# Kernel optimization log

Hardware: AMD Instinct MI355X
Metric: run time of the kernel (lower is better)

## Reference

```python
import jax, jax.numpy as jnp
import numpy as np

N, E, G = 50000, 800000, 128      # nodes, edges, graphs
IN, H, OUT = 128, 128, 2          # feature dims
K, L = 3, 3                       # Chebyshev order, num conv layers
EPS = 1e-5


def setup_inputs() -> dict:
    key = jax.random.key(0)
    ks = jax.random.split(key, 10)
    x = jax.random.normal(ks[0], (N, IN), dtype=jnp.float32)
    edge_index = jax.random.randint(ks[1], (2, E), 0, N, dtype=jnp.int64)
    batch = jnp.sort(jax.random.randint(ks[2], (N,), 0, G, dtype=jnp.int64))
    w_in = jax.random.normal(ks[3], (IN, H), dtype=jnp.float32) * 0.05
    b_in = jnp.zeros((H,), jnp.float32)
    ln_g = jnp.ones((H,), jnp.float32)
    ln_b = jnp.zeros((H,), jnp.float32)
    cheb_w = jax.random.normal(ks[4], (L, K, H, H), dtype=jnp.float32) * 0.05
    cheb_b = jnp.zeros((L, H), jnp.float32)
    bn_g = jnp.ones((L, H), jnp.float32)
    bn_b = jnp.zeros((L, H), jnp.float32)
    w1 = jax.random.normal(ks[5], (H, H // 2), dtype=jnp.float32) * 0.05
    b1 = jnp.zeros((H // 2,), jnp.float32)
    w2 = jax.random.normal(ks[6], (H // 2, OUT), dtype=jnp.float32) * 0.05
    b2 = jnp.zeros((OUT,), jnp.float32)
    return dict(x=x, w_in=w_in, b_in=b_in, ln_g=ln_g, ln_b=ln_b,
                cheb_w=cheb_w, cheb_b=cheb_b, bn_g=bn_g, bn_b=bn_b,
                w1=w1, b1=b1, w2=w2, b2=b2,
                edge_index=edge_index, batch=batch)


def reference(x, w_in, b_in, ln_g, ln_b, cheb_w, cheb_b, bn_g, bn_b,
              w1, b1, w2, b2, edge_index, batch):
    src, dst = edge_index[0], edge_index[1]

    # ChebConv scaled Laplacian with lambda_max=2, sym norm:
    # L_hat = -D^{-1/2} A D^{-1/2}  (self-loop terms cancel in PyG's __norm__)
    deg = jax.ops.segment_sum(jnp.ones((E,), x.dtype), src, num_segments=N)
    dinv = jnp.where(deg > 0, jax.lax.rsqrt(jnp.maximum(deg, 1.0)), 0.0)
    w_edge = -dinv[src] * dinv[dst]  # [E]

    def spmm(h):  # y_i = sum_{(j->i)} w_edge * h_j
        return jax.ops.segment_sum(w_edge[:, None] * h[src], dst, num_segments=N)

    # node_embed: Linear -> LayerNorm -> ReLU (dropout p used in eval => identity)
    h = x @ w_in + b_in
    mu = h.mean(-1, keepdims=True)
    var = h.var(-1, keepdims=True)
    h = (h - mu) * jax.lax.rsqrt(var + EPS) * ln_g + ln_b
    h = jax.nn.relu(h)

    hiddens = [h]
    for l in range(L):
        # Chebyshev recurrence: T0 = h, T1 = L_hat h, Tk = 2 L_hat T_{k-1} - T_{k-2}
        tx0 = h
        out = tx0 @ cheb_w[l, 0]
        tx1 = spmm(tx0)
        out = out + tx1 @ cheb_w[l, 1]
        for k in range(2, K):
            tx2 = 2.0 * spmm(tx1) - tx0
            out = out + tx2 @ cheb_w[l, k]
            tx0, tx1 = tx1, tx2
        out = out + cheb_b[l]
        # BatchNorm1d over nodes (training-mode batch statistics, biased var)
        m = out.mean(0)
        v = out.var(0)
        out = (out - m) * jax.lax.rsqrt(v + EPS) * bn_g[l] + bn_b[l]
        h = jax.nn.relu(out)
        hiddens.append(h)

    # Laplacian (Dirichlet) regularization over all hidden states
    reg = jnp.float32(0.0)
    for hh in hiddens:
        diff = hh[src] - hh[dst]              # [E, H]
        reg = reg + jnp.mean(jnp.sum(diff * diff, axis=-1))
    reg = reg / len(hiddens)

    # global mean pool over batch assignment
    counts = jax.ops.segment_sum(jnp.ones((N,), x.dtype), batch, num_segments=G)
    gsum = jax.ops.segment_sum(h, batch, num_segments=G)
    gmean = gsum / jnp.maximum(counts, 1.0)[:, None]

    z = jax.nn.relu(gmean @ w1 + b1)
    logits = z @ w2 + b2
    return logits, reg
```

## Files before the change

### kernel.cpp

```cpp
#include <hip/hip_runtime.h>
#include <hip/hip_bf16.h>

#define NNODES 50000
#define NEDGES 800000
#define NGRAPH 128
#define EPSV 1e-5f

typedef __attribute__((ext_vector_type(8))) short bf16x8;
typedef __attribute__((ext_vector_type(8))) unsigned short us16x8;
typedef __attribute__((ext_vector_type(4))) float f32x4;
typedef __attribute__((ext_vector_type(2))) float f32x2;

__device__ __forceinline__ unsigned short f2bf(float f) {
    unsigned u = __float_as_uint(f);
    return (unsigned short)((u + 0x7fffu + ((u >> 16) & 1u)) >> 16);
}
__device__ __forceinline__ float bf2f(unsigned short h) {
    return __uint_as_float(((unsigned)h) << 16);
}
__device__ __forceinline__ unsigned pk4_fp8(float a, float b, float c, float d) {
    int w = __builtin_amdgcn_cvt_pk_fp8_f32(a, b, 0, false);
    w = __builtin_amdgcn_cvt_pk_fp8_f32(c, d, w, true);
    return (unsigned)w;
}

__global__ void deg_kernel(const int* __restrict__ src, const int* __restrict__ dst,
                           int* __restrict__ outdeg, int* __restrict__ indeg, int E) {
    int e = blockIdx.x * blockDim.x + threadIdx.x;
    if (e < E) {
        atomicAdd(&outdeg[src[e]], 1);
        atomicAdd(&indeg[dst[e]], 1);
    }
}

__global__ void scan_part(const int* __restrict__ deg, int* __restrict__ bsum,
                          const int* __restrict__ outdeg, float* __restrict__ dinv, int n) {
    __shared__ int sh[256];
    int t = threadIdx.x, i = blockIdx.x * 256 + t;
    if (i < n) {
        int d = outdeg[i];
        dinv[i] = (d > 0) ? rsqrtf((float)d) : 0.0f;
    }
    sh[t] = (i < n) ? deg[i] : 0;
    __syncthreads();
    for (int off = 128; off > 0; off >>= 1) {
        if (t < off) sh[t] += sh[t + off];
        __syncthreads();
    }
    if (t == 0) bsum[blockIdx.x] = sh[0];
}

__global__ void scan_top(int* __restrict__ bsum, int* __restrict__ total, int nb,
                         const int* __restrict__ batch, int* __restrict__ gstart, int n) {
    __shared__ int sh[256];
    int t = threadIdx.x;
    int v = (t < nb) ? bsum[t] : 0;
    sh[t] = v;
    __syncthreads();
    for (int off = 1; off < 256; off <<= 1) {
        int x = (t >= off) ? sh[t - off] : 0;
        __syncthreads();
        sh[t] += x;
        __syncthreads();
    }
    if (t < nb) bsum[t] = sh[t] - v;
    if (t == nb - 1) total[0] = sh[t];
    if (t <= NGRAPH) {
        int lo = 0, hi = n;
        while (lo < hi) {
            int mid = (lo + hi) >> 1;
            if (batch[mid] < t) lo = mid + 1; else hi = mid;
        }
        gstart[t] = lo;
    }
}

__global__ void scan_apply(const int* __restrict__ deg, const int* __restrict__ bsum,
                           int* __restrict__ row_off, int* __restrict__ cursor, int n) {
    __shared__ int sh[256];
    int t = threadIdx.x, i = blockIdx.x * 256 + t;
    int v = (i < n) ? deg[i] : 0;
    sh[t] = v;
    __syncthreads();
    for (int off = 1; off < 256; off <<= 1) {
        int x = (t >= off) ? sh[t - off] : 0;
        __syncthreads();
        sh[t] += x;
        __syncthreads();
    }
    if (i < n) {
        int r = bsum[blockIdx.x] + sh[t] - v;
        row_off[i] = r;
        cursor[i] = r;
    }
}

__global__ void fill_kernel(const int* __restrict__ src, const int* __restrict__ dst,
                            int* __restrict__ cursor, int* __restrict__ col, int E) {
    int e = blockIdx.x * blockDim.x + threadIdx.x;
    if (e < E) {
        int d = dst[e];
        int pos = atomicAdd(&cursor[d], 1);
        col[pos] = src[e];
    }
}

__global__ void wprep_kernel(const float* __restrict__ w_in, const float* __restrict__ cheb_w,
                             unsigned short* __restrict__ Wsp) {
    int p = blockIdx.x;
    int t = threadIdx.x;
    for (int s8 = 0; s8 < 8; ++s8) {
        int slot = s8 * 256 + t;
        int kc = slot >> 9, ct = (slot >> 6) & 7, lane = slot & 63;
        int q = lane >> 4, nn = lane & 15;
        unsigned short* o = Wsp + ((size_t)p * 2048 + slot) * 16;
#pragma unroll
        for (int j = 0; j < 8; ++j) {
            int k = kc * 32 + q * 8 + j, c = ct * 16 + nn;
            float v;
            if (p == 0) {
                v = w_in[k * 128 + c];
            } else {
                int pl = (p - 1) / 3, kk = (p - 1) % 3;
                v = cheb_w[((size_t)(pl * 3 + kk) * 128 + k) * 128 + c];
                if (kk == 0) v -= cheb_w[((size_t)(pl * 3 + 2) * 128 + k) * 128 + c];
                else if (kk == 2) v *= 2.f;
            }
            unsigned short hi = f2bf(v);
            o[j] = hi;
            o[8 + j] = f2bf(v - bf2f(hi));
        }
    }
}

template <int NPARTS, int EPI, int AF32>
__global__ __launch_bounds__(256) void gemm_mfma(
    const void* __restrict__ A0v, const void* __restrict__ A1v, const void* __restrict__ A2v,
    const unsigned short* __restrict__ Wsp, const float* __restrict__ bias,
    float* __restrict__ outp, unsigned short* __restrict__ out16,
    const float* __restrict__ g0, const float* __restrict__ b0,
    float* __restrict__ colsum, float* __restrict__ colsumsq, int n) {
    __shared__ float red[256];
    int t = threadIdx.x, w = t >> 6, l = t & 63;
    int m = l & 15, qk = l >> 4;
    int rowA = blockIdx.x * 64 + w * 16 + m;
    red[t] = 0.f;
    __syncthreads();

    f32x4 acc[8];
#pragma unroll
    for (int ct = 0; ct < 8; ++ct) acc[ct] = (f32x4){0.f, 0.f, 0.f, 0.f};

    bool valid = rowA < n;
#pragma unroll
    for (int p = 0; p < NPARTS; ++p) {
#pragma unroll
        for (int kc = 0; kc < 4; ++kc) {
            bf16x8 ah, al;
            if (AF32) {
                const float* arow = (const float*)A0v;
                if (p == 1) arow = (const float*)A1v;
                if (p == 2) arow = (const float*)A2v;
                arow += (size_t)rowA * 128;
                float4 x0, x1;
                if (valid) {
                    x0 = *(const float4*)&arow[kc * 32 + qk * 8];
                    x1 = *(const float4*)&arow[kc * 32 + qk * 8 + 4];
                } else {
                    x0 = make_float4(0.f, 0.f, 0.f, 0.f); x1 = x0;
                }
                float xs[8] = {x0.x, x0.y, x0.z, x0.w, x1.x, x1.y, x1.z, x1.w};
#pragma unroll
                for (int j = 0; j < 8; ++j) {
                    unsigned short hi = f2bf(xs[j]);
                    ah[j] = (short)hi;
                    al[j] = (short)f2bf(xs[j] - bf2f(hi));
                }
            } else {
                const unsigned short* arow = (const unsigned short*)A0v;
                if (p == 1) arow = (const unsigned short*)A1v;
                if (p == 2) arow = (const unsigned short*)A2v;
                arow += (size_t)rowA * 128;
                if (valid) ah = *(const bf16x8*)&arow[kc * 32 + qk * 8];
                else ah = (bf16x8){0, 0, 0, 0, 0, 0, 0, 0};
            }
            const unsigned short* wb = Wsp + ((size_t)((p * 4 + kc) * 8) * 64 + l) * 16;
#pragma unroll
            for (int ct = 0; ct < 8; ++ct) {
                bf16x8 bh = *(const bf16x8*)(wb + (size_t)ct * 64 * 16);
                bf16x8 bl = *(const bf16x8*)(wb + (size_t)ct * 64 * 16 + 8);
                acc[ct] = __builtin_amdgcn_mfma_f32_16x16x32_bf16(ah, bh, acc[ct], 0, 0, 0);
                if (AF32)
                    acc[ct] = __builtin_amdgcn_mfma_f32_16x16x32_bf16(al, bh, acc[ct], 0, 0, 0);
                acc[ct] = __builtin_amdgcn_mfma_f32_16x16x32_bf16(ah, bl, acc[ct], 0, 0, 0);
            }
        }
    }

    int rowC0 = blockIdx.x * 64 + w * 16 + qk * 4;
    if (EPI == 0) {
        float rs[4] = {0.f, 0.f, 0.f, 0.f}, rss[4] = {0.f, 0.f, 0.f, 0.f};
#pragma unroll
        for (int ct = 0; ct < 8; ++ct) {
            float b = bias[ct * 16 + m];
#pragma unroll
            for (int j = 0; j < 4; ++j) {
                float v = acc[ct][j] + b;
                acc[ct][j] = v;
                rs[j] += v; rss[j] += v * v;
            }
        }
#pragma unroll
        for (int off = 1; off < 16; off <<= 1) {
#pragma unroll
            for (int j = 0; j < 4; ++j) {
                rs[j] += __shfl_xor(rs[j], off, 64);
                rss[j] += __shfl_xor(rss[j], off, 64);
            }
        }
        float mean[4], rstd[4];
#pragma unroll
        for (int j = 0; j < 4; ++j) {
            mean[j] = rs[j] * (1.f / 128.f);
            float var = rss[j] * (1.f / 128.f) - mean[j] * mean[j];
            rstd[j] = rsqrtf(var + EPSV);
        }
#pragma unroll
        for (int ct = 0; ct < 8; ++ct) {
            int c = ct * 16 + m;
            float gg = g0[c], bb = b0[c];
#pragma unroll
            for (int j = 0; j < 4; ++j) {
                int gr = rowC0 + j;
                if (gr < n) {
                    float x = (acc[ct][j] - mean[j]) * rstd[j] * gg + bb;
                    x = fmaxf(x, 0.f);
                    outp[(size_t)gr * 128 + c] = x;
                    out16[(size_t)gr * 128 + c] = f2bf(x);
                }
            }
        }
    } else {
#pragma unroll
        for (int ct = 0; ct < 8; ++ct) {
            int c = ct * 16 + m;
            float b = bias[c];
            float s = 0.f, ss = 0.f;
#pragma unroll
            for (int j = 0; j < 4; ++j) {
                int gr = rowC0 + j;
                if (gr < n) {
                    float v = acc[ct][j] + b;
                    outp[(size_t)gr * 128 + c] = v;
                    s += v; ss += v * v;
                }
            }
            s += __shfl_xor(s, 16, 64);  ss += __shfl_xor(ss, 16, 64);
            s += __shfl_xor(s, 32, 64);  ss += __shfl_xor(ss, 32, 64);
            if (qk == 0) {
                atomicAdd(&red[c], s);
                atomicAdd(&red[128 + c], ss);
            }
        }
        __syncthreads();
        if (t < 128) {
            atomicAdd(&colsum[t], red[t]);
            atomicAdd(&colsumsq[t], red[128 + t]);
        }
    }
}

template <int MODE>
__global__ void spmm_kernel(const unsigned short* __restrict__ g16,
                            const float* __restrict__ self32,
                            unsigned short* __restrict__ dst16, unsigned char* __restrict__ dst8,
                            const int* __restrict__ row_off, const int* __restrict__ col,
                            const float* __restrict__ dinv,
                            const int* __restrict__ outdeg, const int* __restrict__ indeg,
                            int n, double* __restrict__ norm_slots, double* __restrict__ cross_slots) {
    int w = (int)((blockIdx.x * (unsigned)blockDim.x + threadIdx.x) >> 6);
    if (w >= n) return;
    int lane = threadIdx.x & 63;
    int g = lane >> 4;
    int q = lane & 15;
    int s = row_off[w], e = row_off[w + 1];
    float hi[8];
    float4 a = *(const float4*)&self32[(size_t)w * 128 + q * 8];
    float4 b = *(const float4*)&self32[(size_t)w * 128 + q * 8 + 4];
    hi[0] = a.x; hi[1] = a.y; hi[2] = a.z; hi[3] = a.w;
    hi[4] = b.x; hi[5] = b.y; hi[6] = b.z; hi[7] = b.w;
    float acc[8];
#pragma unroll
    for (int j = 0; j < 8; ++j) acc[j] = 0.f;
    float cr = 0.f;
    for (int base = s; base < e; base += 64) {
        int mm = min(e - base, 64);
        int idx = 0; float dv = 0.f;
        if (lane < mm) { idx = col[base + lane]; dv = dinv[idx]; }
        int iters = (mm + 31) >> 5;
        for (int it = 0; it < iters; ++it) {
            int sb = (it << 5) + (g << 3);
            int jj[8]; float dd[8];
#pragma unroll
            for (int u = 0; u < 8; ++u) {
                jj[u] = __shfl(idx, sb + u, 64);
                dd[u] = __shfl(dv, sb + u, 64);
            }
            us16x8 uu[8];
#pragma unroll
            for (int u = 0; u < 8; ++u) {
                uu[u] = (us16x8){0, 0, 0, 0, 0, 0, 0, 0};
                if (sb + u < mm) uu[u] = *(const us16x8*)&g16[(size_t)jj[u] * 128 + q * 8];
            }
#pragma unroll
            for (int u = 0; u < 8; ++u) {
#pragma unroll
                for (int j = 0; j < 8; ++j) {
                    float v = bf2f(uu[u][j]);
                    if (MODE != 2) acc[j] += dd[u] * v;
                    cr += hi[j] * v;
                }
            }
        }
    }
    if (MODE != 2) {
#pragma unroll
        for (int j = 0; j < 8; ++j) {
            acc[j] += __shfl_xor(acc[j], 16, 64);
            acc[j] += __shfl_xor(acc[j], 32, 64);
        }
        if (g == 0) {
            float di = dinv[w];
            float v[8];
            us16x8 o;
#pragma unroll
            for (int j = 0; j < 8; ++j) { v[j] = -di * acc[j]; o[j] = f2bf(v[j]); }
            *(us16x8*)&dst16[(size_t)w * 128 + q * 8] = o;
            uint2 o8;
            o8.x = pk4_fp8(v[0], v[1], v[2], v[3]);
            o8.y = pk4_fp8(v[4], v[5], v[6], v[7]);
            *(uint2*)&dst8[(size_t)w * 128 + q * 8] = o8;
        }
    }
    {
        float nt = 0.f;
#pragma unroll
        for (int j = 0; j < 8; ++j) nt += hi[j] * hi[j];
        nt *= 0.25f;
        for (int off = 32; off > 0; off >>= 1) {
            cr += __shfl_down(cr, off, 64);
            nt += __shfl_down(nt, off, 64);
        }
        if (lane == 0) {
            int slot = w & 255;
            atomicAdd(&cross_slots[slot], (double)cr);
            atomicAdd(&norm_slots[slot], (double)nt * (double)(outdeg[w] + indeg[w]));
        }
    }
}

__global__ void spmm8_kernel(const unsigned char* __restrict__ g8,
                             unsigned short* __restrict__ dst16,
                             const int* __restrict__ row_off, const int* __restrict__ col,
                             const float* __restrict__ dinv, int n) {
    int w = (int)((blockIdx.x * (unsigned)blockDim.x + threadIdx.x) >> 6);
    if (w >= n) return;
    int lane = threadIdx.x & 63;
    int g = lane >> 4;
    int q = lane & 15;
    int s = row_off[w], e = row_off[w + 1];
    float acc[8];
#pragma unroll
    for (int j = 0; j < 8; ++j) acc[j] = 0.f;
    for (int base = s; base < e; base += 64) {
        int mm = min(e - base, 64);
        int idx = 0; float dv = 0.f;
        if (lane < mm) { idx = col[base + lane]; dv = dinv[idx]; }
        int iters = (mm + 31) >> 5;
        for (int it = 0; it < iters; ++it) {
            int sb = (it << 5) + (g << 3);
            int jj[8]; float dd[8];
#pragma unroll
            for (int u = 0; u < 8; ++u) {
                jj[u] = __shfl(idx, sb + u, 64);
                dd[u] = __shfl(dv, sb + u, 64);
            }
            uint2 uu[8];
#pragma unroll
            for (int u = 0; u < 8; ++u) {
                uu[u] = make_uint2(0, 0);
                if (sb + u < mm) uu[u] = *(const uint2*)&g8[(size_t)jj[u] * 128 + q * 8];
            }
#pragma unroll
            for (int u = 0; u < 8; ++u) {
                f32x2 l0 = __builtin_amdgcn_cvt_pk_f32_fp8(uu[u].x, false);
                f32x2 h0 = __builtin_amdgcn_cvt_pk_f32_fp8(uu[u].x, true);
                f32x2 l1 = __builtin_amdgcn_cvt_pk_f32_fp8(uu[u].y, false);
                f32x2 h1 = __builtin_amdgcn_cvt_pk_f32_fp8(uu[u].y, true);
                acc[0] += dd[u] * l0.x; acc[1] += dd[u] * l0.y;
                acc[2] += dd[u] * h0.x; acc[3] += dd[u] * h0.y;
                acc[4] += dd[u] * l1.x; acc[5] += dd[u] * l1.y;
                acc[6] += dd[u] * h1.x; acc[7] += dd[u] * h1.y;
            }
        }
    }
#pragma unroll
    for (int j = 0; j < 8; ++j) {
        acc[j] += __shfl_xor(acc[j], 16, 64);
        acc[j] += __shfl_xor(acc[j], 32, 64);
    }
    if (g == 0) {
        float di = dinv[w];
        us16x8 o;
#pragma unroll
        for (int j = 0; j < 8; ++j) o[j] = f2bf(-di * acc[j]);
        *(us16x8*)&dst16[(size_t)w * 128 + q * 8] = o;
    }
}

__global__ void bnrelu_kernel(const float* __restrict__ outv,
                              const float* __restrict__ colsum, const float* __restrict__ colsumsq,
                              const float* __restrict__ bn_g, const float* __restrict__ bn_b,
                              float* __restrict__ h, unsigned short* __restrict__ h16,
                              int n, int total4) {
    __shared__ float ssc[128], ssh[128];
    int t = threadIdx.x;
    if (t < 128) {
        float m = colsum[t] / (float)n;
        float v = colsumsq[t] / (float)n - m * m;
        float sc = bn_g[t] * rsqrtf(v + EPSV);
        ssc[t] = sc;
        ssh[t] = bn_b[t] - m * sc;
    }
    __syncthreads();
    int i = blockIdx.x * blockDim.x + t;
    if (i >= total4) return;
    float4 o = ((const float4*)outv)[i];
    int c = (i * 4) & 127;
    float4 r;
    r.x = fmaxf(o.x * ssc[c + 0] + ssh[c + 0], 0.f);
    r.y = fmaxf(o.y * ssc[c + 1] + ssh[c + 1], 0.f);
    r.z = fmaxf(o.z * ssc[c + 2] + ssh[c + 2], 0.f);
    r.w = fmaxf(o.w * ssc[c + 3] + ssh[c + 3], 0.f);
    ((float4*)h)[i] = r;
    ushort4 u = make_ushort4(f2bf(r.x), f2bf(r.y), f2bf(r.z), f2bf(r.w));
    ((ushort4*)h16)[i] = u;
}

__global__ void poolmlp_kernel(const float* __restrict__ h, const int* __restrict__ start,
                               const float* __restrict__ w1, const float* __restrict__ b1,
                               const float* __restrict__ w2, const float* __restrict__ b2,
                               const double* __restrict__ norm_slots,
                               const double* __restrict__ cross_slots,
                               float* __restrict__ out) {
    __shared__ float sm[2][128];
    __shared__ float gm[128];
    int g = blockIdx.x, t = threadIdx.x;
    int half = t >> 7, c = t & 127;
    int s = start[g], e = start[g + 1];
    float acc = 0.f;
    for (int r = s + half; r < e; r += 2) acc += h[(size_t)r * 128 + c];
    sm[half][c] = acc;
    __syncthreads();
    if (t < 128) {
        float cnt = fmaxf((float)(e - s), 1.f);
        gm[t] = (sm[0][t] + sm[1][t]) / cnt;
    }
    __syncthreads();
    if (t < 64) {
        float z = b1[t];
        for (int k = 0; k < 128; ++k) z += gm[k] * w1[(size_t)k * 64 + t];
        z = fmaxf(z, 0.f);
        float p0 = z * w2[t * 2 + 0];
        float p1 = z * w2[t * 2 + 1];
        for (int off = 32; off > 0; off >>= 1) {
            p0 += __shfl_down(p0, off, 64);
            p1 += __shfl_down(p1, off, 64);
        }
        if (t == 0) {
            out[g * 2 + 0] = p0 + b2[0];
            out[g * 2 + 1] = p1 + b2[1];
        }
    } else if (g == 0 && t < 128) {
        int l = t - 64;
        double ns = 0.0, cs = 0.0;
        for (int i = l; i < 256; i += 64) { ns += norm_slots[i]; cs += cross_slots[i]; }
        for (int off = 32; off > 0; off >>= 1) {
            ns += __shfl_down(ns, off, 64);
            cs += __shfl_down(cs, off, 64);
        }
        if (l == 0) out[256] = (float)((ns - 2.0 * cs) / ((double)NEDGES * 4.0));
    }
}

extern "C" void kernel_launch(void* const* d_in, const int* in_sizes, int n_in,
                              void* d_out, int out_size, void* d_ws, size_t ws_size,
                              hipStream_t stream) {
    const float* x      = (const float*)d_in[0];
    const float* w_in   = (const float*)d_in[1];
    const float* b_in   = (const float*)d_in[2];
    const float* ln_g   = (const float*)d_in[3];
    const float* ln_b   = (const float*)d_in[4];
    const float* cheb_w = (const float*)d_in[5];
    const float* cheb_b = (const float*)d_in[6];
    const float* bn_g   = (const float*)d_in[7];
    const float* bn_b   = (const float*)d_in[8];
    const float* w1     = (const float*)d_in[9];
    const float* b1     = (const float*)d_in[10];
    const float* w2     = (const float*)d_in[11];
    const float* b2     = (const float*)d_in[12];
    const int*   eidx   = (const int*)d_in[13];
    const int*   batch  = (const int*)d_in[14];
    const int* src = eidx;
    const int* dst = eidx + NEDGES;
    float* out = (float*)d_out;

    char* ws = (char*)d_ws;
    size_t off = 0;
    auto alloc = [&](size_t bytes) -> void* {
        void* p = ws + off;
        off = (off + bytes + 255) & ~(size_t)255;
        return p;
    };
    float* h    = (float*)alloc((size_t)NNODES * 128 * 4);
    float* ob   = (float*)alloc((size_t)NNODES * 128 * 4);
    unsigned short* h16  = (unsigned short*)alloc((size_t)NNODES * 128 * 2);
    unsigned short* t116 = (unsigned short*)alloc((size_t)NNODES * 128 * 2);
    unsigned short* s16  = (unsigned short*)alloc((size_t)NNODES * 128 * 2);
    unsigned char*  t18  = (unsigned char*)alloc((size_t)NNODES * 128);
    unsigned short* Wsp  = (unsigned short*)alloc((size_t)10 * 2048 * 16 * 2);
    int* degs     = (int*)alloc((size_t)2 * NNODES * 4);
    int* outdeg   = degs;
    int* indeg    = degs + NNODES;
    float* dinv   = (float*)alloc((size_t)NNODES * 4);
    int* row_off  = (int*)alloc((size_t)(NNODES + 1) * 4);
    int* cursor   = (int*)alloc((size_t)NNODES * 4);
    int* colv     = (int*)alloc((size_t)NEDGES * 4);
    int* bsum     = (int*)alloc(256 * 4);
    int* gstart   = (int*)alloc((size_t)(NGRAPH + 1) * 4);
    float* colstats = (float*)alloc(256 * 4);
    double* slots   = (double*)alloc(512 * 8);
    double* norm_slots  = slots;
    double* cross_slots = slots + 256;
    float* colsum = colstats, *colsumsq = colstats + 128;

    hipMemsetAsync(degs, 0, (size_t)2 * NNODES * 4, stream);
    hipMemsetAsync(slots, 0, 512 * 8, stream);

    int tE = (NEDGES + 255) / 256;
    int nb = (NNODES + 255) / 256;
    deg_kernel<<<tE, 256, 0, stream>>>(src, dst, outdeg, indeg, NEDGES);
    scan_part<<<nb, 256, 0, stream>>>(indeg, bsum, outdeg, dinv, NNODES);
    scan_top<<<1, 256, 0, stream>>>(bsum, row_off + NNODES, nb, batch, gstart, NNODES);
    scan_apply<<<nb, 256, 0, stream>>>(indeg, bsum, row_off, cursor, NNODES);
    fill_kernel<<<tE, 256, 0, stream>>>(src, dst, cursor, colv, NEDGES);
    wprep_kernel<<<10, 256, 0, stream>>>(w_in, cheb_w, Wsp);

    int gemmBlocks = (NNODES + 63) / 64;
    int waveBlocks = (NNODES * 64 + 255) / 256;
    int total4 = NNODES * 128 / 4;

    gemm_mfma<1, 0, 1><<<gemmBlocks, 256, 0, stream>>>(x, nullptr, nullptr, Wsp, b_in, h, h16,
                                                       ln_g, ln_b, nullptr, nullptr, NNODES);

    for (int l = 0; l < 3; ++l) {
        hipMemsetAsync(colstats, 0, 256 * 4, stream);
        spmm_kernel<0><<<waveBlocks, 256, 0, stream>>>(h16, h, t116, t18, row_off, colv, dinv,
                                                       outdeg, indeg, NNODES, norm_slots, cross_slots);
        spmm8_kernel<<<waveBlocks, 256, 0, stream>>>(t18, s16, row_off, colv, dinv, NNODES);
        gemm_mfma<3, 1, 0><<<gemmBlocks, 256, 0, stream>>>(h16, t116, s16,
            Wsp + (size_t)(1 + 3 * l) * 2048 * 16, cheb_b + (size_t)l * 128, ob, nullptr,
            nullptr, nullptr, colsum, colsumsq, NNODES);
        bnrelu_kernel<<<(total4 + 255) / 256, 256, 0, stream>>>(ob, colsum, colsumsq,
            bn_g + (size_t)l * 128, bn_b + (size_t)l * 128, h, h16, NNODES, total4);
    }
    spmm_kernel<2><<<waveBlocks, 256, 0, stream>>>(h16, h, nullptr, nullptr, row_off, colv, dinv,
                                                   outdeg, indeg, NNODES, norm_slots, cross_slots);

    poolmlp_kernel<<<NGRAPH, 256, 0, stream>>>(h, gstart, w1, b1, w2, b2,
                                               norm_slots, cross_slots, out);
}
```

Before: 848.2 us.

## Gather fp8 hidden states in SpMM, drop fp32 h, pack dinv into CSR

The first SpMM of each layer and the final regularization pass now gather neighbor rows from a new fp8 copy of h instead of bf16, which halves the gather bytes. Both SpMM passes now share one templated kernel. The fp32 copy of h is removed: the self features, pooling and regularization read bf16, and bnrelu writes bf16 plus fp8. The CSR stores (src, dinv[src]) pairs so the dependent dinv lookup goes away, and the per-layer colstats memsets are merged into one. The cost is lower precision in the Chebyshev T1 term and in the Dirichlet regularization, plus an extra repack kernel after the input embedding.

```diff
diff --git a/kernel.cpp b/kernel.cpp
--- a/kernel.cpp
+++ b/kernel.cpp
@@ -96,12 +96,14 @@
 }
 
 __global__ void fill_kernel(const int* __restrict__ src, const int* __restrict__ dst,
-                            int* __restrict__ cursor, int* __restrict__ col, int E) {
+                            const float* __restrict__ dinv,
+                            int* __restrict__ cursor, int2* __restrict__ colw, int E) {
     int e = blockIdx.x * blockDim.x + threadIdx.x;
     if (e < E) {
+        int s = src[e];
         int d = dst[e];
         int pos = atomicAdd(&cursor[d], 1);
-        col[pos] = src[e];
+        colw[pos] = make_int2(s, __float_as_int(dinv[s]));
     }
 }
 
@@ -235,7 +237,6 @@
                 if (gr < n) {
                     float x = (acc[ct][j] - mean[j]) * rstd[j] * gg + bb;
                     x = fmaxf(x, 0.f);
-                    outp[(size_t)gr * 128 + c] = x;
                     out16[(size_t)gr * 128 + c] = f2bf(x);
                 }
             }
@@ -270,14 +271,25 @@
     }
 }
 
+__global__ void repack8_kernel(const unsigned short* __restrict__ h16,
+                               unsigned char* __restrict__ h8, int total8) {
+    int i = blockIdx.x * blockDim.x + threadIdx.x;
+    if (i >= total8) return;
+    us16x8 a = ((const us16x8*)h16)[i];
+    uint2 o;
+    o.x = pk4_fp8(bf2f(a[0]), bf2f(a[1]), bf2f(a[2]), bf2f(a[3]));
+    o.y = pk4_fp8(bf2f(a[4]), bf2f(a[5]), bf2f(a[6]), bf2f(a[7]));
+    ((uint2*)h8)[i] = o;
+}
+
 template <int MODE>
-__global__ void spmm_kernel(const unsigned short* __restrict__ g16,
-                            const float* __restrict__ self32,
-                            unsigned short* __restrict__ dst16, unsigned char* __restrict__ dst8,
-                            const int* __restrict__ row_off, const int* __restrict__ col,
-                            const float* __restrict__ dinv,
-                            const int* __restrict__ outdeg, const int* __restrict__ indeg,
-                            int n, double* __restrict__ norm_slots, double* __restrict__ cross_slots) {
+__global__ void spmm_g(const unsigned char* __restrict__ g8,
+                       const unsigned short* __restrict__ self16,
+                       unsigned short* __restrict__ dst16, unsigned char* __restrict__ dst8,
+                       const int* __restrict__ row_off, const int2* __restrict__ colw,
+                       const float* __restrict__ dinv,
+                       const int* __restrict__ outdeg, const int* __restrict__ indeg,
+                       int n, double* __restrict__ norm_slots, double* __restrict__ cross_slots) {
     int w = (int)((blockIdx.x * (unsigned)blockDim.x + threadIdx.x) >> 6);
     if (w >= n) return;
     int lane = threadIdx.x & 63;
@@ -285,10 +297,11 @@
     int q = lane & 15;
     int s = row_off[w], e = row_off[w + 1];
     float hi[8];
-    float4 a = *(const float4*)&self32[(size_t)w * 128 + q * 8];
-    float4 b = *(const float4*)&self32[(size_t)w * 128 + q * 8 + 4];
-    hi[0] = a.x; hi[1] = a.y; hi[2] = a.z; hi[3] = a.w;
-    hi[4] = b.x; hi[5] = b.y; hi[6] = b.z; hi[7] = b.w;
+    if (MODE != 1) {
+        us16x8 a = *(const us16x8*)&self16[(size_t)w * 128 + q * 8];
+#pragma unroll
+        for (int j = 0; j < 8; ++j) hi[j] = bf2f(a[j]);
+    }
     float acc[8];
 #pragma unroll
     for (int j = 0; j < 8; ++j) acc[j] = 0.f;
@@ -296,7 +309,11 @@
     for (int base = s; base < e; base += 64) {
         int mm = min(e - base, 64);
         int idx = 0; float dv = 0.f;
-        if (lane < mm) { idx = col[base + lane]; dv = dinv[idx]; }
+        if (lane < mm) {
+            int2 cw = colw[base + lane];
+            idx = cw.x;
+            dv = __int_as_float(cw.y);
+        }
         int iters = (mm + 31) >> 5;
         for (int it = 0; it < iters; ++it) {
             int sb = (it << 5) + (g << 3);
@@ -306,19 +323,26 @@
                 jj[u] = __shfl(idx, sb + u, 64);
                 dd[u] = __shfl(dv, sb + u, 64);
             }
-            us16x8 uu[8];
+            uint2 uu[8];
 #pragma unroll
             for (int u = 0; u < 8; ++u) {
-                uu[u] = (us16x8){0, 0, 0, 0, 0, 0, 0, 0};
-                if (sb + u < mm) uu[u] = *(const us16x8*)&g16[(size_t)jj[u] * 128 + q * 8];
+                uu[u] = make_uint2(0, 0);
+                if (sb + u < mm) uu[u] = *(const uint2*)&g8[(size_t)jj[u] * 128 + q * 8];
             }
 #pragma unroll
             for (int u = 0; u < 8; ++u) {
-#pragma unroll
-                for (int j = 0; j < 8; ++j) {
-                    float v = bf2f(uu[u][j]);
-                    if (MODE != 2) acc[j] += dd[u] * v;
-                    cr += hi[j] * v;
+                f32x2 l0 = __builtin_amdgcn_cvt_pk_f32_fp8(uu[u].x, false);
+                f32x2 h0 = __builtin_amdgcn_cvt_pk_f32_fp8(uu[u].x, true);
+                f32x2 l1 = __builtin_amdgcn_cvt_pk_f32_fp8(uu[u].y, false);
+                f32x2 h1 = __builtin_amdgcn_cvt_pk_f32_fp8(uu[u].y, true);
+                float v[8] = {l0.x, l0.y, h0.x, h0.y, l1.x, l1.y, h1.x, h1.y};
+                if (MODE != 2) {
+#pragma unroll
+                    for (int j = 0; j < 8; ++j) acc[j] += dd[u] * v[j];
+                }
+                if (MODE != 1) {
+#pragma unroll
+                    for (int j = 0; j < 8; ++j) cr += hi[j] * v[j];
                 }
             }
         }
@@ -336,13 +360,15 @@
 #pragma unroll
             for (int j = 0; j < 8; ++j) { v[j] = -di * acc[j]; o[j] = f2bf(v[j]); }
             *(us16x8*)&dst16[(size_t)w * 128 + q * 8] = o;
-            uint2 o8;
-            o8.x = pk4_fp8(v[0], v[1], v[2], v[3]);
-            o8.y = pk4_fp8(v[4], v[5], v[6], v[7]);
-            *(uint2*)&dst8[(size_t)w * 128 + q * 8] = o8;
-        }
-    }
-    {
+            if (MODE == 0) {
+                uint2 o8;
+                o8.x = pk4_fp8(v[0], v[1], v[2], v[3]);
+                o8.y = pk4_fp8(v[4], v[5], v[6], v[7]);
+                *(uint2*)&dst8[(size_t)w * 128 + q * 8] = o8;
+            }
+        }
+    }
+    if (MODE != 1) {
         float nt = 0.f;
 #pragma unroll
         for (int j = 0; j < 8; ++j) nt += hi[j] * hi[j];
@@ -359,69 +385,10 @@
     }
 }
 
-__global__ void spmm8_kernel(const unsigned char* __restrict__ g8,
-                             unsigned short* __restrict__ dst16,
-                             const int* __restrict__ row_off, const int* __restrict__ col,
-                             const float* __restrict__ dinv, int n) {
-    int w = (int)((blockIdx.x * (unsigned)blockDim.x + threadIdx.x) >> 6);
-    if (w >= n) return;
-    int lane = threadIdx.x & 63;
-    int g = lane >> 4;
-    int q = lane & 15;
-    int s = row_off[w], e = row_off[w + 1];
-    float acc[8];
-#pragma unroll
-    for (int j = 0; j < 8; ++j) acc[j] = 0.f;
-    for (int base = s; base < e; base += 64) {
-        int mm = min(e - base, 64);
-        int idx = 0; float dv = 0.f;
-        if (lane < mm) { idx = col[base + lane]; dv = dinv[idx]; }
-        int iters = (mm + 31) >> 5;
-        for (int it = 0; it < iters; ++it) {
-            int sb = (it << 5) + (g << 3);
-            int jj[8]; float dd[8];
-#pragma unroll
-            for (int u = 0; u < 8; ++u) {
-                jj[u] = __shfl(idx, sb + u, 64);
-                dd[u] = __shfl(dv, sb + u, 64);
-            }
-            uint2 uu[8];
-#pragma unroll
-            for (int u = 0; u < 8; ++u) {
-                uu[u] = make_uint2(0, 0);
-                if (sb + u < mm) uu[u] = *(const uint2*)&g8[(size_t)jj[u] * 128 + q * 8];
-            }
-#pragma unroll
-            for (int u = 0; u < 8; ++u) {
-                f32x2 l0 = __builtin_amdgcn_cvt_pk_f32_fp8(uu[u].x, false);
-                f32x2 h0 = __builtin_amdgcn_cvt_pk_f32_fp8(uu[u].x, true);
-                f32x2 l1 = __builtin_amdgcn_cvt_pk_f32_fp8(uu[u].y, false);
-                f32x2 h1 = __builtin_amdgcn_cvt_pk_f32_fp8(uu[u].y, true);
-                acc[0] += dd[u] * l0.x; acc[1] += dd[u] * l0.y;
-                acc[2] += dd[u] * h0.x; acc[3] += dd[u] * h0.y;
-                acc[4] += dd[u] * l1.x; acc[5] += dd[u] * l1.y;
-                acc[6] += dd[u] * h1.x; acc[7] += dd[u] * h1.y;
-            }
-        }
-    }
-#pragma unroll
-    for (int j = 0; j < 8; ++j) {
-        acc[j] += __shfl_xor(acc[j], 16, 64);
-        acc[j] += __shfl_xor(acc[j], 32, 64);
-    }
-    if (g == 0) {
-        float di = dinv[w];
-        us16x8 o;
-#pragma unroll
-        for (int j = 0; j < 8; ++j) o[j] = f2bf(-di * acc[j]);
-        *(us16x8*)&dst16[(size_t)w * 128 + q * 8] = o;
-    }
-}
-
 __global__ void bnrelu_kernel(const float* __restrict__ outv,
                               const float* __restrict__ colsum, const float* __restrict__ colsumsq,
                               const float* __restrict__ bn_g, const float* __restrict__ bn_b,
-                              float* __restrict__ h, unsigned short* __restrict__ h16,
+                              unsigned short* __restrict__ h16, unsigned char* __restrict__ h8,
                               int n, int total4) {
     __shared__ float ssc[128], ssh[128];
     int t = threadIdx.x;
@@ -442,12 +409,12 @@
     r.y = fmaxf(o.y * ssc[c + 1] + ssh[c + 1], 0.f);
     r.z = fmaxf(o.z * ssc[c + 2] + ssh[c + 2], 0.f);
     r.w = fmaxf(o.w * ssc[c + 3] + ssh[c + 3], 0.f);
-    ((float4*)h)[i] = r;
     ushort4 u = make_ushort4(f2bf(r.x), f2bf(r.y), f2bf(r.z), f2bf(r.w));
     ((ushort4*)h16)[i] = u;
-}
-
-__global__ void poolmlp_kernel(const float* __restrict__ h, const int* __restrict__ start,
+    ((unsigned*)h8)[i] = pk4_fp8(r.x, r.y, r.z, r.w);
+}
+
+__global__ void poolmlp_kernel(const unsigned short* __restrict__ h16, const int* __restrict__ start,
                                const float* __restrict__ w1, const float* __restrict__ b1,
                                const float* __restrict__ w2, const float* __restrict__ b2,
                                const double* __restrict__ norm_slots,
@@ -459,7 +426,7 @@
     int half = t >> 7, c = t & 127;
     int s = start[g], e = start[g + 1];
     float acc = 0.f;
-    for (int r = s + half; r < e; r += 2) acc += h[(size_t)r * 128 + c];
+    for (int r = s + half; r < e; r += 2) acc += bf2f(h16[(size_t)r * 128 + c]);
     sm[half][c] = acc;
     __syncthreads();
     if (t < 128) {
@@ -522,11 +489,11 @@
         off = (off + bytes + 255) & ~(size_t)255;
         return p;
     };
-    float* h    = (float*)alloc((size_t)NNODES * 128 * 4);
     float* ob   = (float*)alloc((size_t)NNODES * 128 * 4);
     unsigned short* h16  = (unsigned short*)alloc((size_t)NNODES * 128 * 2);
     unsigned short* t116 = (unsigned short*)alloc((size_t)NNODES * 128 * 2);
     unsigned short* s16  = (unsigned short*)alloc((size_t)NNODES * 128 * 2);
+    unsigned char*  h8   = (unsigned char*)alloc((size_t)NNODES * 128);
     unsigned char*  t18  = (unsigned char*)alloc((size_t)NNODES * 128);
     unsigned short* Wsp  = (unsigned short*)alloc((size_t)10 * 2048 * 16 * 2);
     int* degs     = (int*)alloc((size_t)2 * NNODES * 4);
@@ -535,17 +502,16 @@
     float* dinv   = (float*)alloc((size_t)NNODES * 4);
     int* row_off  = (int*)alloc((size_t)(NNODES + 1) * 4);
     int* cursor   = (int*)alloc((size_t)NNODES * 4);
-    int* colv     = (int*)alloc((size_t)NEDGES * 4);
+    int2* colw    = (int2*)alloc((size_t)NEDGES * 8);
     int* bsum     = (int*)alloc(256 * 4);
     int* gstart   = (int*)alloc((size_t)(NGRAPH + 1) * 4);
-    float* colstats = (float*)alloc(256 * 4);
-    double* slots   = (double*)alloc(512 * 8);
+    float* colstats = (float*)alloc(768 * 4 + 512 * 8);
+    double* slots   = (double*)(colstats + 768);
     double* norm_slots  = slots;
     double* cross_slots = slots + 256;
-    float* colsum = colstats, *colsumsq = colstats + 128;
 
     hipMemsetAsync(degs, 0, (size_t)2 * NNODES * 4, stream);
-    hipMemsetAsync(slots, 0, 512 * 8, stream);
+    hipMemsetAsync(colstats, 0, 768 * 4 + 512 * 8, stream);
 
     int tE = (NEDGES + 255) / 256;
     int nb = (NNODES + 255) / 256;
@@ -553,30 +519,35 @@
     scan_part<<<nb, 256, 0, stream>>>(indeg, bsum, outdeg, dinv, NNODES);
     scan_top<<<1, 256, 0, stream>>>(bsum, row_off + NNODES, nb, batch, gstart, NNODES);
     scan_apply<<<nb, 256, 0, stream>>>(indeg, bsum, row_off, cursor, NNODES);
-    fill_kernel<<<tE, 256, 0, stream>>>(src, dst, cursor, colv, NEDGES);
+    fill_kernel<<<tE, 256, 0, stream>>>(src, dst, dinv, cursor, colw, NEDGES);
     wprep_kernel<<<10, 256, 0, stream>>>(w_in, cheb_w, Wsp);
 
     int gemmBlocks = (NNODES + 63) / 64;
     int waveBlocks = (NNODES * 64 + 255) / 256;
     int total4 = NNODES * 128 / 4;
-
-    gemm_mfma<1, 0, 1><<<gemmBlocks, 256, 0, stream>>>(x, nullptr, nullptr, Wsp, b_in, h, h16,
+    int total8 = NNODES * 128 / 8;
+
+    gemm_mfma<1, 0, 1><<<gemmBlocks, 256, 0, stream>>>(x, nullptr, nullptr, Wsp, b_in,
+                                                       nullptr, h16,
                                                        ln_g, ln_b, nullptr, nullptr, NNODES);
+    repack8_kernel<<<(total8 + 255) / 256, 256, 0, stream>>>(h16, h8, total8);
 
     for (int l = 0; l < 3; ++l) {
-        hipMemsetAsync(colstats, 0, 256 * 4, stream);
-        spmm_kernel<0><<<waveBlocks, 256, 0, stream>>>(h16, h, t116, t18, row_off, colv, dinv,
-                                                       outdeg, indeg, NNODES, norm_slots, cross_slots);
-        spmm8_kernel<<<waveBlocks, 256, 0, stream>>>(t18, s16, row_off, colv, dinv, NNODES);
+        float* colsum = colstats + 256 * l;
+        float* colsumsq = colsum + 128;
+        spmm_g<0><<<waveBlocks, 256, 0, stream>>>(h8, h16, t116, t18, row_off, colw, dinv,
+                                                  outdeg, indeg, NNODES, norm_slots, cross_slots);
+        spmm_g<1><<<waveBlocks, 256, 0, stream>>>(t18, nullptr, s16, nullptr, row_off, colw, dinv,
+                                                  outdeg, indeg, NNODES, nullptr, nullptr);
         gemm_mfma<3, 1, 0><<<gemmBlocks, 256, 0, stream>>>(h16, t116, s16,
             Wsp + (size_t)(1 + 3 * l) * 2048 * 16, cheb_b + (size_t)l * 128, ob, nullptr,
             nullptr, nullptr, colsum, colsumsq, NNODES);
         bnrelu_kernel<<<(total4 + 255) / 256, 256, 0, stream>>>(ob, colsum, colsumsq,
-            bn_g + (size_t)l * 128, bn_b + (size_t)l * 128, h, h16, NNODES, total4);
-    }
-    spmm_kernel<2><<<waveBlocks, 256, 0, stream>>>(h16, h, nullptr, nullptr, row_off, colv, dinv,
-                                                   outdeg, indeg, NNODES, norm_slots, cross_slots);
-
-    poolmlp_kernel<<<NGRAPH, 256, 0, stream>>>(h, gstart, w1, b1, w2, b2,
+            bn_g + (size_t)l * 128, bn_b + (size_t)l * 128, h16, h8, NNODES, total4);
+    }
+    spmm_g<2><<<waveBlocks, 256, 0, stream>>>(h8, h16, nullptr, nullptr, row_off, colw, dinv,
+                                              outdeg, indeg, NNODES, norm_slots, cross_slots);
+
+    poolmlp_kernel<<<NGRAPH, 256, 0, stream>>>(h16, gstart, w1, b1, w2, b2,
                                                norm_slots, cross_slots, out);
 }
```

Result: faster. 794.8 us (-6.3%).
